# Kernel tuning notes

Hardware: AMD Instinct MI355X
Metric: run time of the kernel (lower is better)

Reference implementation:

```python
import jax, jax.numpy as jnp
import numpy as np

B, S, F, H = 4, 1024, 256, 8
SCALE = float(F) ** 0.5  # source MULTIPLIES logits by sqrt(f)


def setup_inputs() -> dict:
    key = jax.random.key(0)
    ks = jax.random.split(key, 5)
    # 0.02 init scale keeps sigmoid logits in a non-saturated range
    return {
        "q_input": jax.random.normal(ks[0], (B, S, F), dtype=jnp.float32),
        "Wq": jax.random.normal(ks[1], (F, F * H), dtype=jnp.float32) * 0.02,
        "Wk": jax.random.normal(ks[2], (F, F * H), dtype=jnp.float32) * 0.02,
        "Wv": jax.random.normal(ks[3], (F, F * H), dtype=jnp.float32) * 0.02,
        "Wo": jax.random.normal(ks[4], (F * H, F), dtype=jnp.float32) * 0.02,
    }


def reference(q_input, Wq, Wk, Wv, Wo):
    b, s, f = q_input.shape
    h = Wq.shape[1] // f
    # kv_input is None in source -> self-attention (kv = q_input)
    q = (q_input.reshape(b * s, f) @ Wq).reshape(b, s, f, h)
    k = (q_input.reshape(b * s, f) @ Wk).reshape(b, s, f, h)
    v = (q_input.reshape(b * s, f) @ Wv).reshape(b, s, f, h)
    qkt = jnp.einsum('bifh,bjfh->bijh', q, k)          # [b, i, j, h]
    attn = jax.nn.sigmoid(qkt * SCALE)                  # sigmoid, NOT softmax
    wv = jnp.einsum('bijh,bjfh->bifh', attn, v)         # [b, i, f, h]
    wv = wv.reshape(b * s, f * h)
    out = jax.nn.relu(wv @ Wo)                          # projection + ReLU
    return out.reshape(b, s, f)
```

## Files before the change

kernel.cpp:

```cpp
#include <hip/hip_runtime.h>
#include <math.h>

#define SQ 1024
#define FQ 256
#define FH 2048

typedef _Float16 f16;
typedef f16  f16x8 __attribute__((ext_vector_type(8)));
typedef f16  f16x4 __attribute__((ext_vector_type(4)));
typedef float f32x4 __attribute__((ext_vector_type(4)));

#define GLOAD_LDS16(gp, lp) \
    __builtin_amdgcn_global_load_lds((const __attribute__((address_space(1))) void*)(gp), \
                                     (__attribute__((address_space(3))) void*)(lp), 16, 0, 0)

#define SIG16(s) __builtin_amdgcn_rcpf(1.0f + __builtin_amdgcn_exp2f(-23.083120654223414f * (s)))

__global__ __launch_bounds__(256) void prep_kernel(const float* __restrict__ x,
                                                   const float* __restrict__ Wq,
                                                   const float* __restrict__ Wk,
                                                   const float* __restrict__ Wv,
                                                   const float* __restrict__ Wo,
                                                   f16* __restrict__ xh,
                                                   f16* __restrict__ wqT,
                                                   f16* __restrict__ wkT,
                                                   f16* __restrict__ wvT,
                                                   f16* __restrict__ woT) {
    const int z = blockIdx.z;
    if (z == 4) {
        int id = (int)(blockIdx.x * 8 + blockIdx.y);
        int idx = (id * 256 + (int)threadIdx.x) * 8;
        float4 a = *(const float4*)(x + idx);
        float4 b = *(const float4*)(x + idx + 4);
        f16x8 v = {(f16)a.x, (f16)a.y, (f16)a.z, (f16)a.w,
                   (f16)b.x, (f16)b.y, (f16)b.z, (f16)b.w};
        *(f16x8*)(xh + idx) = v;
        return;
    }
    __shared__ f16 T[32][33];
    const int tx = threadIdx.x & 31, ty = threadIdx.x >> 5;
    if (z < 3) {
        const float* W = z == 0 ? Wq : (z == 1 ? Wk : Wv);
        f16* WT        = z == 0 ? wqT : (z == 1 ? wkT : wvT);
        const int n0 = blockIdx.x * 32, k0 = blockIdx.y * 32;
#pragma unroll
        for (int i = 0; i < 4; ++i)
            T[ty + i * 8][tx] = (f16)W[(size_t)(k0 + ty + i * 8) * FH + n0 + tx];
        __syncthreads();
#pragma unroll
        for (int i = 0; i < 4; ++i)
            WT[(size_t)(n0 + ty + i * 8) * FQ + k0 + tx] = T[tx][ty + i * 8];
    } else {
        const int n0 = (blockIdx.x >> 3) * 32;
        const int yy = (blockIdx.x & 7) * 8 + blockIdx.y;
        const int ft = yy >> 3, h = yy & 7;
#pragma unroll
        for (int i = 0; i < 4; ++i) {
            int fl = ty + i * 8;
            T[fl][tx] = (f16)Wo[(size_t)((ft * 32 + fl) * 8 + h) * FQ + n0 + tx];
        }
        __syncthreads();
#pragma unroll
        for (int i = 0; i < 4; ++i)
            woT[(size_t)(n0 + ty + i * 8) * FH + h * 256 + ft * 32 + tx] = T[tx][ty + i * 8];
    }
}

__device__ __forceinline__ void stage_sw64(const f16* __restrict__ G, int ldg,
                                           int row0, int c0, f16* S,
                                           int nrows, int w, int lane) {
    const int rsub = lane >> 3;
    const int g    = (lane & 7) ^ (rsub & 7);
#pragma unroll
    for (int rI = w; rI < (nrows >> 3); rI += 4) {
        GLOAD_LDS16(G + (size_t)(row0 + rI * 8 + rsub) * ldg + c0 + g * 8,
                    S + rI * 512);
    }
}

__device__ __forceinline__ void gemm128_sw(const f16* __restrict__ A, int lda,
                                           const f16* __restrict__ Bt, int ldb,
                                           int kbeg, int kend, f16* As, f16* Bs,
                                           f32x4 acc[4][4], int row0, int col0) {
    const int t = threadIdx.x, lane = t & 63, w = t >> 6;
    const int wr = w >> 1, wc = w & 1;
    const int lrow = lane & 15, quad = lane >> 4;
    for (int k0 = kbeg; k0 < kend; k0 += 64) {
        __syncthreads();
        stage_sw64(A, lda, row0, k0, As, 128, w, lane);
        stage_sw64(Bt, ldb, col0, k0, Bs, 128, w, lane);
        __syncthreads();
#pragma unroll
        for (int kk = 0; kk < 2; ++kk) {
            f16x8 af[4], bf[4];
#pragma unroll
            for (int i = 0; i < 4; ++i) {
                int r = wr * 64 + i * 16 + lrow;
                af[i] = *(const f16x8*)&As[r * 64 + (((kk * 4 + quad) ^ (r & 7)) << 3)];
            }
#pragma unroll
            for (int j = 0; j < 4; ++j) {
                int r = wc * 64 + j * 16 + lrow;
                bf[j] = *(const f16x8*)&Bs[r * 64 + (((kk * 4 + quad) ^ (r & 7)) << 3)];
            }
#pragma unroll
            for (int i = 0; i < 4; ++i)
#pragma unroll
                for (int j = 0; j < 4; ++j)
                    acc[i][j] = __builtin_amdgcn_mfma_f32_16x16x32_f16(af[i], bf[j], acc[i][j], 0, 0, 0);
        }
    }
}

__global__ __launch_bounds__(256) void proj_mfma(const f16* __restrict__ xh,
                                                 const f16* __restrict__ wqT,
                                                 const f16* __restrict__ wkT,
                                                 const f16* __restrict__ wvT,
                                                 f16* __restrict__ qb,
                                                 f16* __restrict__ kb,
                                                 f16* __restrict__ vb) {
    const int z = blockIdx.z;
    const f16* WT = z == 0 ? wqT : (z == 1 ? wkT : wvT);
    f16* O        = z == 0 ? qb  : (z == 1 ? kb  : vb);
    __shared__ f16 smem[17408];
    f16* As = smem;
    f16* Bs = smem + 8192;
    f32x4 acc[4][4] = {};
    const int row0 = blockIdx.y * 128, col0 = blockIdx.x * 128;
    gemm128_sw(xh, FQ, WT, FQ, 0, FQ, As, Bs, acc, row0, col0);

    __syncthreads();
    f16* Es = smem;
    const int lane = threadIdx.x & 63, w = threadIdx.x >> 6;
    const int wr = w >> 1, wc = w & 1;
    const int lrow = lane & 15, quad = lane >> 4;
    if (z != 2) {
#pragma unroll
        for (int i = 0; i < 4; ++i)
#pragma unroll
            for (int rr = 0; rr < 4; ++rr) {
                int rl = 64 * wr + 16 * i + 4 * quad + rr;
#pragma unroll
                for (int j = 0; j < 4; ++j) {
                    int cc = 64 * wc + 16 * j + lrow;
                    Es[rl * 136 + (cc & 7) * 16 + (cc >> 3)] = (f16)acc[i][j][rr];
                }
            }
        __syncthreads();
        const int f0 = col0 >> 3;
#pragma unroll
        for (int it = 0; it < 4; ++it) {
            int c = it * 256 + threadIdx.x;
            int row = c >> 3, hh = c & 7;
            int gr = row0 + row, bbb = gr >> 10, s = gr & 1023;
            f16x8 v0 = *(const f16x8*)&Es[row * 136 + hh * 16];
            f16x8 v1 = *(const f16x8*)&Es[row * 136 + hh * 16 + 8];
            f16* dst = O + ((size_t)(bbb * 8 + hh) * SQ + s) * FQ + f0;
            *(f16x8*)dst = v0;
            *(f16x8*)(dst + 8) = v1;
        }
    } else {
#pragma unroll
        for (int i = 0; i < 4; ++i)
#pragma unroll
            for (int rr = 0; rr < 4; ++rr) {
                int rl = 64 * wr + 16 * i + 4 * quad + rr;
#pragma unroll
                for (int j = 0; j < 4; ++j) {
                    int cc = 64 * wc + 16 * j + lrow;
                    Es[cc * 136 + rl] = (f16)acc[i][j][rr];
                }
            }
        __syncthreads();
        const int bbb = row0 >> 10, s0 = row0 & 1023;
#pragma unroll
        for (int it = 0; it < 8; ++it) {
            int c = it * 256 + threadIdx.x;
            int cc = c >> 4, sc = c & 15;
            int hh = cc & 7, f = (col0 >> 3) + (cc >> 3);
            f16x8 v = *(const f16x8*)&Es[cc * 136 + sc * 8];
            *(f16x8*)(O + ((size_t)(bbb * 8 + hh) * FQ + f) * SQ + s0 + sc * 8) = v;
        }
    }
}

__global__ __launch_bounds__(512, 2) void fused_attn(const f16* __restrict__ Qb,
                                                     const f16* __restrict__ Kb,
                                                     const f16* __restrict__ Vt,
                                                     f16* __restrict__ WV) {
    __shared__ f16 smem[75776];
    const int t = threadIdx.x, lane = t & 63, w = t >> 6;
    const int grp = w >> 2, wl = w & 3;
    const int lrow = lane & 15, quad = lane >> 4;
    f16* Pw = smem + 65536 + w * 1280;
    const int n = blockIdx.x;
    const int xcd = n & 7, rest = n >> 3;
    const int bh = xcd * 4 + (rest & 3);
    const int strip = rest >> 2;
    const int m0 = strip * 128;
    const int bb = bh >> 3, h = bh & 7;
    const f16* Qg = Qb + (size_t)bh * SQ * FQ;
    const f16* Kg = Kb + (size_t)bh * SQ * FQ;
    const f16* Vg = Vt + (size_t)bh * FQ * SQ;

    f16x8 qf[2][8];
#pragma unroll
    for (int mi = 0; mi < 2; ++mi)
#pragma unroll
        for (int ks = 0; ks < 8; ++ks)
            qf[mi][ks] = *(const f16x8*)(Qg + (size_t)(m0 + 32 * wl + 16 * mi + lrow) * FQ
                                             + ks * 32 + quad * 8);

    const int krs = lane >> 5;
    const int kgp = lane & 31;
    const int vrs = lane >> 2;
    const int vgp = lane & 3;

    if (grp == 0) {
#pragma unroll
        for (int kt = 0; kt < 2; ++kt)
#pragma unroll
            for (int i = 0; i < 4; ++i) {
                int rI = wl + i * 4;
                int r = rI * 2 + krs;
                GLOAD_LDS16(Kg + (size_t)(kt * 32 + r) * FQ + ((kgp ^ (r & 7)) << 3),
                            smem + kt * 8192 + rI * 512);
            }
    } else {
#pragma unroll
        for (int kt = 0; kt < 2; ++kt)
#pragma unroll
            for (int i = 0; i < 4; ++i) {
                int rI = wl + i * 4;
                int f = rI * 16 + vrs;
                GLOAD_LDS16(Vg + (size_t)f * SQ + kt * 32 + ((vgp ^ ((f >> 1) & 3)) << 3),
                            smem + 32768 + kt * 8192 + rI * 512);
            }
    }

    f32x4 acc_o[2][16] = {};

    for (int it = 0; it < 16; ++it) {
        const int p = it & 1;
        f16* KBc = smem + (p * 2 + grp) * 8192;
        f16* VBc = smem + 32768 + (p * 2 + grp) * 8192;
        __syncthreads();
        if (it < 15) {
            const int pn = p ^ 1;
            const int base = (it + 1) * 64;
            if (grp == 0) {
#pragma unroll
                for (int kt = 0; kt < 2; ++kt)
#pragma unroll
                    for (int i = 0; i < 4; ++i) {
                        int rI = wl + i * 4;
                        int r = rI * 2 + krs;
                        GLOAD_LDS16(Kg + (size_t)(base + kt * 32 + r) * FQ + ((kgp ^ (r & 7)) << 3),
                                    smem + (pn * 2 + kt) * 8192 + rI * 512);
                    }
            } else {
#pragma unroll
                for (int kt = 0; kt < 2; ++kt)
#pragma unroll
                    for (int i = 0; i < 4; ++i) {
                        int rI = wl + i * 4;
                        int f = rI * 16 + vrs;
                        GLOAD_LDS16(Vg + (size_t)f * SQ + base + kt * 32 + ((vgp ^ ((f >> 1) & 3)) << 3),
                                    smem + 32768 + (pn * 2 + kt) * 8192 + rI * 512);
                    }
            }
        }
        f32x4 acc_s[2][2] = {};
#pragma unroll
        for (int ks = 0; ks < 8; ++ks) {
            f16x8 bf[2];
#pragma unroll
            for (int nj = 0; nj < 2; ++nj) {
                int rk = 16 * nj + lrow;
                bf[nj] = *(const f16x8*)&KBc[rk * 256 + (((ks * 4 + quad) ^ (rk & 7)) << 3)];
            }
#pragma unroll
            for (int nj = 0; nj < 2; ++nj)
#pragma unroll
                for (int mi = 0; mi < 2; ++mi)
                    acc_s[nj][mi] = __builtin_amdgcn_mfma_f32_16x16x32_f16(
                        bf[nj], qf[mi][ks], acc_s[nj][mi], 0, 0, 0);
        }
#pragma unroll
        for (int nj = 0; nj < 2; ++nj)
#pragma unroll
            for (int mi = 0; mi < 2; ++mi) {
                f16x4 v;
#pragma unroll
                for (int rr = 0; rr < 4; ++rr)
                    v[rr] = (f16)SIG16(acc_s[nj][mi][rr]);
                *(f16x4*)&Pw[(16 * mi + lrow) * 40 + 16 * nj + 4 * quad] = v;
            }
        f16x8 ap[2];
#pragma unroll
        for (int mi = 0; mi < 2; ++mi)
            ap[mi] = *(const f16x8*)&Pw[(16 * mi + lrow) * 40 + quad * 8];
        __builtin_amdgcn_s_setprio(1);
#pragma unroll
        for (int nj = 0; nj < 16; ++nj) {
            int f = 16 * nj + lrow;
            f16x8 bv = *(const f16x8*)&VBc[f * 32 + ((quad ^ ((f >> 1) & 3)) << 3)];
#pragma unroll
            for (int mi = 0; mi < 2; ++mi)
                acc_o[mi][nj] = __builtin_amdgcn_mfma_f32_16x16x32_f16(
                    ap[mi], bv, acc_o[mi][nj], 0, 0, 0);
        }
        __builtin_amdgcn_s_setprio(0);
    }
    __syncthreads();
    float* Fb = (float*)(smem + 34816);
    f16* Es = smem;
#pragma unroll
    for (int mi = 0; mi < 2; ++mi) {
        if (grp == 1) {
#pragma unroll
            for (int nj = 0; nj < 16; ++nj)
                *(f32x4*)&Fb[((wl * 16 + nj) << 8) + lane * 4] = acc_o[mi][nj];
        }
        __syncthreads();
        if (grp == 0) {
#pragma unroll
            for (int nj = 0; nj < 16; ++nj) {
                f32x4 s = acc_o[mi][nj] +
                          *(const f32x4*)&Fb[((wl * 16 + nj) << 8) + lane * 4];
#pragma unroll
                for (int rr = 0; rr < 4; ++rr)
                    Es[(32 * wl + 16 * mi + 4 * quad + rr) * 264 + 16 * nj + lrow] =
                        (f16)s[rr];
            }
        }
        __syncthreads();
    }
#pragma unroll
    for (int it = 0; it < 8; ++it) {
        int c = it * 512 + t;
        int r = c >> 5, ck = c & 31;
        f16x8 v = *(const f16x8*)&Es[r * 264 + ck * 8];
        *(f16x8*)(WV + (size_t)(bb * SQ + m0 + r) * FH + h * 256 + ck * 8) = v;
    }
}

__global__ __launch_bounds__(256) void out_mfma4(const f16* __restrict__ WVm,
                                                 const f16* __restrict__ WoT,
                                                 float* __restrict__ PP) {
    __shared__ f16 smem[16384];
    f16* As = smem;
    f16* Bs = smem + 8192;
    f32x4 acc[4][4] = {};
    const int row0 = blockIdx.y * 128, col0 = blockIdx.x * 128;
    const int kbeg = blockIdx.z * 512;
    gemm128_sw(WVm, FH, WoT, FH, kbeg, kbeg + 512, As, Bs, acc, row0, col0);

    float* P = PP + (size_t)blockIdx.z * SQ * 4 * FQ;
    const int lane = threadIdx.x & 63, w = threadIdx.x >> 6;
    const int wr = w >> 1, wc = w & 1;
    const int lrow = lane & 15, quad = lane >> 4;
#pragma unroll
    for (int i = 0; i < 4; ++i)
#pragma unroll
        for (int rr = 0; rr < 4; ++rr) {
            int gr = row0 + wr * 64 + i * 16 + quad * 4 + rr;
#pragma unroll
            for (int j = 0; j < 4; ++j) {
                int gc = col0 + wc * 64 + j * 16 + lrow;
                P[(size_t)gr * FQ + gc] = acc[i][j][rr];
            }
        }
}

__global__ __launch_bounds__(256) void reduce_relu4(const float* __restrict__ PP,
                                                    float* __restrict__ O) {
    int idx = (blockIdx.x * 256 + threadIdx.x) * 4;
    f32x4 s = *(const f32x4*)(PP + idx);
#pragma unroll
    for (int z = 1; z < 4; ++z)
        s += *(const f32x4*)(PP + (size_t)z * 1048576 + idx);
    f32x4 r = {fmaxf(s.x, 0.f), fmaxf(s.y, 0.f), fmaxf(s.z, 0.f), fmaxf(s.w, 0.f)};
    *(f32x4*)(O + idx) = r;
}

extern "C" void kernel_launch(void* const* d_in, const int* in_sizes, int n_in,
                              void* d_out, int out_size, void* d_ws, size_t ws_size,
                              hipStream_t stream) {
    const float* x  = (const float*)d_in[0];
    const float* Wq = (const float*)d_in[1];
    const float* Wk = (const float*)d_in[2];
    const float* Wv = (const float*)d_in[3];
    const float* Wo = (const float*)d_in[4];
    float* out = (float*)d_out;

    f16* ws = (f16*)d_ws;
    f16* xh    = ws;
    f16* wqT   = xh    + 1048576;
    f16* wkT   = wqT   + 524288;
    f16* wvT   = wkT   + 524288;
    f16* woT   = wvT   + 524288;
    f16* qbuf  = woT   + 524288;
    f16* kbuf  = qbuf  + 8388608;
    f16* vbuf  = kbuf  + 8388608;
    f16* wvbuf = vbuf  + 8388608;
    float* pp  = (float*)qbuf;

    dim3 blk(256);
    prep_kernel<<<dim3(64, 8, 5), blk, 0, stream>>>(x, Wq, Wk, Wv, Wo,
                                                    xh, wqT, wkT, wvT, woT);

    proj_mfma<<<dim3(16, 32, 3), blk, 0, stream>>>(xh, wqT, wkT, wvT, qbuf, kbuf, vbuf);

    fused_attn<<<dim3(256), dim3(512), 0, stream>>>(qbuf, kbuf, vbuf, wvbuf);

    out_mfma4<<<dim3(2, 32, 4), blk, 0, stream>>>(wvbuf, woT, pp);
    reduce_relu4<<<dim3(1024), blk, 0, stream>>>(pp, out);
}
```

Baseline: 160.6 us.

## Switch attention to 32x32x16 MFMA and pass probabilities via permlane swap

Rewrites the fused attention inner loop to use 32x32x16 MFMA tiles instead of 16x16x32 for both the QK^T and PV products. The sigmoid probabilities are packed with cvt_pkrtz and rearranged into the A-operand layout in registers using permlane32_swap, which removes the per-wave LDS staging buffer and its round trip. The epilogue reduction is reworked for the new accumulator layout. Larger tiles cut LDS reads per FLOP, at the cost of higher register pressure from the 16-wide accumulators and a gfx950-specific intrinsic.

Measured after the change: 162.2 us. No clear change (+1.0%).

```diff
diff --git a/kernel.cpp b/kernel.cpp
--- a/kernel.cpp
+++ b/kernel.cpp
@@ -8,7 +8,10 @@
 typedef _Float16 f16;
 typedef f16  f16x8 __attribute__((ext_vector_type(8)));
 typedef f16  f16x4 __attribute__((ext_vector_type(4)));
+typedef __fp16 fp16x2 __attribute__((ext_vector_type(2)));
 typedef float f32x4 __attribute__((ext_vector_type(4)));
+typedef float f32x16 __attribute__((ext_vector_type(16)));
+typedef unsigned uint2v __attribute__((ext_vector_type(2)));
 
 #define GLOAD_LDS16(gp, lp) \
     __builtin_amdgcn_global_load_lds((const __attribute__((address_space(1))) void*)(gp), \
@@ -188,11 +191,10 @@
                                                      const f16* __restrict__ Kb,
                                                      const f16* __restrict__ Vt,
                                                      f16* __restrict__ WV) {
-    __shared__ f16 smem[75776];
+    __shared__ f16 smem[67584];
     const int t = threadIdx.x, lane = t & 63, w = t >> 6;
     const int grp = w >> 2, wl = w & 3;
-    const int lrow = lane & 15, quad = lane >> 4;
-    f16* Pw = smem + 65536 + w * 1280;
+    const int l31 = lane & 31, hf = lane >> 5;
     const int n = blockIdx.x;
     const int xcd = n & 7, rest = n >> 3;
     const int bh = xcd * 4 + (rest & 3);
@@ -203,13 +205,10 @@
     const f16* Kg = Kb + (size_t)bh * SQ * FQ;
     const f16* Vg = Vt + (size_t)bh * FQ * SQ;
 
-    f16x8 qf[2][8];
-#pragma unroll
-    for (int mi = 0; mi < 2; ++mi)
-#pragma unroll
-        for (int ks = 0; ks < 8; ++ks)
-            qf[mi][ks] = *(const f16x8*)(Qg + (size_t)(m0 + 32 * wl + 16 * mi + lrow) * FQ
-                                             + ks * 32 + quad * 8);
+    f16x8 qf[16];
+#pragma unroll
+    for (int ks = 0; ks < 16; ++ks)
+        qf[ks] = *(const f16x8*)(Qg + (size_t)(m0 + 32 * wl + l31) * FQ + ks * 16 + hf * 8);
 
     const int krs = lane >> 5;
     const int kgp = lane & 31;
@@ -238,7 +237,7 @@
             }
     }
 
-    f32x4 acc_o[2][16] = {};
+    f32x16 acc_o[8] = {};
 
     for (int it = 0; it < 16; ++it) {
         const int p = it & 1;
@@ -270,68 +269,74 @@
                     }
             }
         }
-        f32x4 acc_s[2][2] = {};
-#pragma unroll
-        for (int ks = 0; ks < 8; ++ks) {
-            f16x8 bf[2];
-#pragma unroll
-            for (int nj = 0; nj < 2; ++nj) {
-                int rk = 16 * nj + lrow;
-                bf[nj] = *(const f16x8*)&KBc[rk * 256 + (((ks * 4 + quad) ^ (rk & 7)) << 3)];
-            }
-#pragma unroll
-            for (int nj = 0; nj < 2; ++nj)
-#pragma unroll
-                for (int mi = 0; mi < 2; ++mi)
-                    acc_s[nj][mi] = __builtin_amdgcn_mfma_f32_16x16x32_f16(
-                        bf[nj], qf[mi][ks], acc_s[nj][mi], 0, 0, 0);
-        }
-#pragma unroll
-        for (int nj = 0; nj < 2; ++nj)
-#pragma unroll
-            for (int mi = 0; mi < 2; ++mi) {
-                f16x4 v;
-#pragma unroll
-                for (int rr = 0; rr < 4; ++rr)
-                    v[rr] = (f16)SIG16(acc_s[nj][mi][rr]);
-                *(f16x4*)&Pw[(16 * mi + lrow) * 40 + 16 * nj + 4 * quad] = v;
-            }
-        f16x8 ap[2];
-#pragma unroll
-        for (int mi = 0; mi < 2; ++mi)
-            ap[mi] = *(const f16x8*)&Pw[(16 * mi + lrow) * 40 + quad * 8];
-        __builtin_amdgcn_s_setprio(1);
-#pragma unroll
-        for (int nj = 0; nj < 16; ++nj) {
-            int f = 16 * nj + lrow;
-            f16x8 bv = *(const f16x8*)&VBc[f * 32 + ((quad ^ ((f >> 1) & 3)) << 3)];
-#pragma unroll
-            for (int mi = 0; mi < 2; ++mi)
-                acc_o[mi][nj] = __builtin_amdgcn_mfma_f32_16x16x32_f16(
-                    ap[mi], bv, acc_o[mi][nj], 0, 0, 0);
-        }
-        __builtin_amdgcn_s_setprio(0);
+        f32x16 acc_s = {};
+#pragma unroll
+        for (int ks = 0; ks < 16; ++ks) {
+            int pg = (2 * ks + hf) ^ (l31 & 7);
+            f16x8 af = *(const f16x8*)&KBc[l31 * 256 + (pg << 3)];
+            acc_s = __builtin_amdgcn_mfma_f32_32x32x16_f16(af, qf[ks], acc_s, 0, 0, 0);
+        }
+        f16x8 pa0, pa1;
+        {
+            unsigned wpk[8];
+#pragma unroll
+            for (int i = 0; i < 8; ++i) {
+                fp16x2 pk = __builtin_amdgcn_cvt_pkrtz(SIG16(acc_s[2 * i]),
+                                                       SIG16(acc_s[2 * i + 1]));
+                wpk[i] = __builtin_bit_cast(unsigned, pk);
+            }
+            uint2v r0 = __builtin_amdgcn_permlane32_swap(wpk[0], wpk[2], false, false);
+            uint2v r1 = __builtin_amdgcn_permlane32_swap(wpk[1], wpk[3], false, false);
+            uint2v r2 = __builtin_amdgcn_permlane32_swap(wpk[4], wpk[6], false, false);
+            uint2v r3 = __builtin_amdgcn_permlane32_swap(wpk[5], wpk[7], false, false);
+            union { unsigned u[4]; f16x8 v; } u0, u1;
+            u0.u[0] = r0[0]; u0.u[1] = r1[0]; u0.u[2] = r0[1]; u0.u[3] = r1[1];
+            u1.u[0] = r2[0]; u1.u[1] = r3[0]; u1.u[2] = r2[1]; u1.u[3] = r3[1];
+            pa0 = u0.v;
+            pa1 = u1.v;
+        }
+#pragma unroll
+        for (int nt = 0; nt < 8; ++nt) {
+            int f = 32 * nt + l31;
+            int sw = (f >> 1) & 3;
+            f16x8 bv0 = *(const f16x8*)&VBc[f * 32 + ((hf ^ sw) << 3)];
+            f16x8 bv1 = *(const f16x8*)&VBc[f * 32 + (((2 + hf) ^ sw) << 3)];
+            acc_o[nt] = __builtin_amdgcn_mfma_f32_32x32x16_f16(pa0, bv0, acc_o[nt], 0, 0, 0);
+            acc_o[nt] = __builtin_amdgcn_mfma_f32_32x32x16_f16(pa1, bv1, acc_o[nt], 0, 0, 0);
+        }
     }
     __syncthreads();
     float* Fb = (float*)(smem + 34816);
     f16* Es = smem;
 #pragma unroll
-    for (int mi = 0; mi < 2; ++mi) {
+    for (int np = 0; np < 2; ++np) {
         if (grp == 1) {
 #pragma unroll
-            for (int nj = 0; nj < 16; ++nj)
-                *(f32x4*)&Fb[((wl * 16 + nj) << 8) + lane * 4] = acc_o[mi][nj];
+            for (int nt4 = 0; nt4 < 4; ++nt4) {
+                int nt = np * 4 + nt4;
+#pragma unroll
+                for (int r2 = 0; r2 < 4; ++r2) {
+                    f32x4 c = {acc_o[nt][4 * r2], acc_o[nt][4 * r2 + 1],
+                               acc_o[nt][4 * r2 + 2], acc_o[nt][4 * r2 + 3]};
+                    *(f32x4*)&Fb[(((wl * 4 + nt4) * 4 + r2) << 8) + lane * 4] = c;
+                }
+            }
         }
         __syncthreads();
         if (grp == 0) {
 #pragma unroll
-            for (int nj = 0; nj < 16; ++nj) {
-                f32x4 s = acc_o[mi][nj] +
-                          *(const f32x4*)&Fb[((wl * 16 + nj) << 8) + lane * 4];
-#pragma unroll
-                for (int rr = 0; rr < 4; ++rr)
-                    Es[(32 * wl + 16 * mi + 4 * quad + rr) * 264 + 16 * nj + lrow] =
-                        (f16)s[rr];
+            for (int nt4 = 0; nt4 < 4; ++nt4) {
+                int nt = np * 4 + nt4;
+#pragma unroll
+                for (int r2 = 0; r2 < 4; ++r2) {
+                    f32x4 own = {acc_o[nt][4 * r2], acc_o[nt][4 * r2 + 1],
+                                 acc_o[nt][4 * r2 + 2], acc_o[nt][4 * r2 + 3]};
+                    f32x4 s = own + *(const f32x4*)&Fb[(((wl * 4 + nt4) * 4 + r2) << 8) + lane * 4];
+#pragma unroll
+                    for (int rr = 0; rr < 4; ++rr)
+                        Es[(32 * wl + rr + 8 * r2 + 4 * hf) * 264 + 32 * nt + l31] =
+                            (f16)s[rr];
+                }
             }
         }
         __syncthreads();
```
